# Kernel optimization log

Measured on AMD Instinct MI355X. Metric: run time of the kernel, lower is better.

## Reference

```python
import jax, jax.numpy as jnp
import numpy as np

N = 50000      # nodes
E = 800000     # edges per graph set
D_IN = 128
D_H = 128
NG = 64        # graphs in batch


def gcn(x, W, b, src, dst, w):
    # PyG GCNConv: add self loops (weight 1), symmetric normalization, then
    # out[i] = sum_{(j->i)} norm_ji * (x @ W)[j] + b
    h = x @ W                                   # [N, Dh]
    loop = jnp.arange(N)
    s = jnp.concatenate([src, loop])
    d = jnp.concatenate([dst, loop])
    ww = jnp.concatenate([w, jnp.ones((N,), w.dtype)])
    deg = jax.ops.segment_sum(ww, d, num_segments=N)
    dis = jnp.where(deg > 0, jax.lax.rsqrt(deg), 0.0)
    norm = dis[s] * ww * dis[d]                 # [E+N]
    out = jax.ops.segment_sum(h[s] * norm[:, None], d, num_segments=N)
    return out + b


def setup_inputs() -> dict:
    key = jax.random.key(0)
    ks = jax.random.split(key, 16)
    inp = {
        "edge_index1": jax.random.randint(ks[0], (2, E), 0, N),
        "edge_weight1": jax.random.uniform(ks[1], (E,), jnp.float32),
        "edge_index2": jax.random.randint(ks[2], (2, E), 0, N),
        "edge_weight2": jax.random.uniform(ks[3], (E,), jnp.float32),
        "fm0": jax.random.normal(ks[4], (N, D_IN), jnp.float32),
        "fm1": jax.random.normal(ks[5], (N, D_IN), jnp.float32),
        "batch_tensor": jnp.sort(jax.random.randint(ks[6], (N,), 0, NG)),
        # params (torch Linear stored transposed as [in, out])
        "W1": jax.random.normal(ks[7], (D_IN, D_H), jnp.float32) / np.sqrt(D_IN),
        "b1": jnp.zeros((D_H,), jnp.float32),
        "W2": jax.random.normal(ks[8], (D_H, D_H), jnp.float32) / np.sqrt(D_H),
        "b2": jnp.zeros((D_H,), jnp.float32),
        "M1w": jax.random.normal(ks[9], (D_H, D_H), jnp.float32) / np.sqrt(D_H),
        "M1b": jnp.zeros((D_H,), jnp.float32),
        "M2w": jax.random.normal(ks[10], (D_H, D_H // 2), jnp.float32) / np.sqrt(D_H),
        "M2b": jnp.zeros((D_H // 2,), jnp.float32),
        "M3w": jax.random.normal(ks[11], (D_H // 2, D_H // 4), jnp.float32) / np.sqrt(D_H // 2),
        "M3b": jnp.zeros((D_H // 4,), jnp.float32),
        "M4w": jax.random.normal(ks[12], (D_H // 4, 1), jnp.float32) / np.sqrt(D_H // 4),
        "M4b": jnp.zeros((1,), jnp.float32),
    }
    return inp


def reference(edge_index1, edge_weight1, edge_index2, edge_weight2, fm0, fm1,
              batch_tensor, W1, b1, W2, b2, M1w, M1b, M2w, M2b, M3w, M3b, M4w, M4b):
    s1, d1 = edge_index1[0], edge_index1[1]
    s2, d2 = edge_index2[0], edge_index2[1]
    x11 = gcn(fm0, W1, b1, s1, d1, edge_weight1)
    x12 = gcn(fm1, W1, b1, s2, d2, edge_weight2)
    x21 = gcn(x11, W2, b2, s1, d1, edge_weight1)
    x22 = gcn(x12, W2, b2, s2, d2, edge_weight2)
    x = (x12 - x11) * (x22 - x21)               # [N, Dh]
    # global mean pool by graph id
    sums = jax.ops.segment_sum(x, batch_tensor, num_segments=NG)
    cnt = jax.ops.segment_sum(jnp.ones((N,), x.dtype), batch_tensor, num_segments=NG)
    g = sums / jnp.maximum(cnt, 1.0)[:, None]   # [NG, Dh]
    # MLP (dropout = identity at inference; no activations in original)
    h = g @ M1w + M1b
    h = h @ M2w + M2b
    h = h @ M3w + M3b
    return h @ M4w + M4b                        # [NG, 1]
```

## Files before the change

kernel.cpp:

```cpp
#include <hip/hip_runtime.h>
#include <hip/hip_fp16.h>

#define N_NODES 50000
#define N_EDGES 800000
#define NGRAPH 64
#define PCHUNK 16
#define NRANGE 8
#define RSPAN 6250
#define ECHUNK 2048
#define NCHK ((N_EDGES + ECHUNK - 1) / ECHUNK)
#define AGG_NB 782
#define CAP 48

typedef _Float16 half8 __attribute__((ext_vector_type(8)));
typedef float f32x4 __attribute__((ext_vector_type(4)));

#define GSTRH ((size_t)N_NODES * 128)
#define CCH ((size_t)N_NODES * 32)

__device__ __forceinline__ float pk_w(unsigned p) {
  return __half2float(__ushort_as_half((unsigned short)(p >> 16)));
}
__device__ __forceinline__ unsigned pk_src(unsigned p) { return p & 0xFFFFu; }

__global__ __launch_bounds__(256) void curinit_kernel(
    int* __restrict__ cur1, int* __restrict__ cur2) {
  int i = blockIdx.x * 256 + threadIdx.x;
  if (i < N_NODES) {
    cur1[i] = i * CAP;
    cur2[i] = i * CAP;
  }
}

__global__ __launch_bounds__(256) void fill_kernel(
    const int* __restrict__ ei1, const float* __restrict__ w1,
    int* __restrict__ cur1, unsigned* __restrict__ ec1,
    const int* __restrict__ ei2, const float* __restrict__ w2,
    int* __restrict__ cur2, unsigned* __restrict__ ec2) {
  int r = blockIdx.x & 7, chunk = blockIdx.x >> 3;
  unsigned lo = r * RSPAN;
  int base = chunk * ECHUNK + threadIdx.x;
#pragma unroll
  for (int k = 0; k < ECHUNK / 256; ++k) {
    int e = base + k * 256;
    if (e < N_EDGES) {
      unsigned d1 = (unsigned)__builtin_nontemporal_load(&ei1[N_EDGES + e]);
      if (d1 - lo < RSPAN) {
        int s = __builtin_nontemporal_load(&ei1[e]);
        float w = __builtin_nontemporal_load(&w1[e]);
        int slot = atomicAdd(&cur1[d1], 1);
        if (slot < (int)(d1 * CAP + CAP))
          ec1[slot] = (unsigned)s |
                      ((unsigned)__half_as_ushort(__float2half(w)) << 16);
      }
      unsigned d2 = (unsigned)__builtin_nontemporal_load(&ei2[N_EDGES + e]);
      if (d2 - lo < RSPAN) {
        int s = __builtin_nontemporal_load(&ei2[e]);
        float w = __builtin_nontemporal_load(&w2[e]);
        int slot = atomicAdd(&cur2[d2], 1);
        if (slot < (int)(d2 * CAP + CAP))
          ec2[slot] = (unsigned)s |
                      ((unsigned)__half_as_ushort(__float2half(w)) << 16);
      }
    }
  }
}

__global__ __launch_bounds__(256) void degdis_kernel(
    const int* __restrict__ cn1, const unsigned* __restrict__ ec1,
    const int* __restrict__ cn2, const unsigned* __restrict__ ec2,
    float* __restrict__ dis1, float* __restrict__ dis2) {
  int i = blockIdx.x * 256 + threadIdx.x;
  if (i >= 2 * N_NODES) return;
  const int* cn;
  const unsigned* ec;
  float* dis;
  int node;
  if (i < N_NODES) { cn = cn1; ec = ec1; dis = dis1; node = i; }
  else { cn = cn2; ec = ec2; dis = dis2; node = i - N_NODES; }
  int beg = node * CAP;
  int end = min(cn[node], beg + CAP);
  float s = 1.0f;
  for (int e = beg; e < end; ++e) s += pk_w(ec[e]);
  dis[node] = rsqrtf(s);
}

template <bool XF16>
__global__ __launch_bounds__(256) void gemm_mfma_kernel(
    const void* __restrict__ X0v, const void* __restrict__ X1v,
    const float* __restrict__ W,
    const float* __restrict__ dis1, const float* __restrict__ dis2,
    __half* __restrict__ Y) {
  __shared__ half8 wfrag[4][8][64];
  int tid = threadIdx.x;
  for (int ent = tid; ent < 4 * 8 * 64; ent += 256) {
    int lane = ent & 63, nt = (ent >> 6) & 7, kk = ent >> 9;
    int kbase = kk * 32 + (lane >> 4) * 8;
    int n = nt * 16 + (lane & 15);
    half8 hv;
#pragma unroll
    for (int j = 0; j < 8; ++j) hv[j] = (_Float16)W[(kbase + j) * 128 + n];
    wfrag[kk][nt][lane] = hv;
  }
  __syncthreads();
  int wv = tid >> 6, lane = tid & 63;
  int row0 = blockIdx.x * 64 + wv * 16;
  int arow = row0 + (lane & 15);
  int ar = (arow < 2 * N_NODES) ? arow : 0;
  f32x4 acc[8] = {};
#pragma unroll
  for (int kk = 0; kk < 4; ++kk) {
    int sub = lane >> 4;
    half8 af;
    if constexpr (XF16) {
      int gg = ar >= N_NODES;
      int nd = ar - gg * N_NODES;
      const __half* xs = (const __half*)X0v + (size_t)gg * GSTRH +
                         (size_t)kk * CCH + (size_t)nd * 32 + sub * 8;
      af = *(const half8*)xs;
    } else {
      int kb = kk * 32 + sub * 8;
      const float* xs = (ar < N_NODES)
                            ? ((const float*)X0v + (size_t)ar * 128)
                            : ((const float*)X1v + (size_t)(ar - N_NODES) * 128);
      float4 xa = *(const float4*)(xs + kb);
      float4 xb = *(const float4*)(xs + kb + 4);
      af[0] = (_Float16)xa.x; af[1] = (_Float16)xa.y;
      af[2] = (_Float16)xa.z; af[3] = (_Float16)xa.w;
      af[4] = (_Float16)xb.x; af[5] = (_Float16)xb.y;
      af[6] = (_Float16)xb.z; af[7] = (_Float16)xb.w;
    }
#pragma unroll
    for (int nt = 0; nt < 8; ++nt)
      acc[nt] = __builtin_amdgcn_mfma_f32_16x16x32_f16(af, wfrag[kk][nt][lane],
                                                       acc[nt], 0, 0, 0);
  }
#pragma unroll
  for (int rg = 0; rg < 4; ++rg) {
    int r = row0 + ((lane >> 4) * 4) + rg;
    if (r < 2 * N_NODES) {
      int gg = r >= N_NODES;
      int nd = r - gg * N_NODES;
      float d = gg ? dis2[nd] : dis1[nd];
#pragma unroll
      for (int nt = 0; nt < 8; ++nt)
        Y[(size_t)gg * GSTRH + (size_t)(nt >> 1) * CCH + (size_t)nd * 32 +
          (nt & 1) * 16 + (lane & 15)] = __float2half(d * acc[nt][rg]);
    }
  }
}

__global__ __launch_bounds__(256) void aggregate_kernel(
    const int* __restrict__ cn1, const unsigned* __restrict__ ec1,
    const float* __restrict__ dis1,
    const int* __restrict__ cn2, const unsigned* __restrict__ ec2,
    const float* __restrict__ dis2,
    const __half* __restrict__ H, const float* __restrict__ bias,
    __half* __restrict__ out) {
  int tid = threadIdx.x;
  int combo = blockIdx.x & 7;
  int nb = blockIdx.x >> 3;
  int g = combo >> 2;
  int c = combo & 3;
  int l = tid & 63, w = tid >> 6;
  int node = nb * 64 + w * 16 + (l >> 2);
  int flane = l & 3;
  if (node >= N_NODES) return;
  const int* cn = g ? cn2 : cn1;
  const unsigned* ec = g ? ec2 : ec1;
  const float* dis = g ? dis2 : dis1;
  const float4* T4 = (const float4*)(H + (size_t)g * GSTRH + (size_t)c * CCH);
  float2 a[4];
  a[0] = a[1] = a[2] = a[3] = make_float2(0.f, 0.f);
  int beg = node * CAP;
  int end = min(cn[node], beg + CAP);
  for (int e = beg; e < end; e += 8) {
#pragma unroll
    for (int k = 0; k < 8; ++k) {
      if (e + k < end) {
        unsigned p = ec[e + k];
        float cw = pk_w(p);
        float4 raw = T4[(size_t)pk_src(p) * 4 + flane];
        const __half2* hp = (const __half2*)&raw;
#pragma unroll
        for (int q = 0; q < 4; ++q) {
          float2 hv = __half22float2(hp[q]);
          a[q].x += cw * hv.x;
          a[q].y += cw * hv.y;
        }
      }
    }
  }
  float d = dis[node];
  float4 sraw = T4[(size_t)node * 4 + flane];
  const __half2* sp = (const __half2*)&sraw;
  __half2 o[4];
#pragma unroll
  for (int q = 0; q < 4; ++q) {
    float2 sv = __half22float2(sp[q]);
    float2 bz = *(const float2*)&bias[c * 32 + flane * 8 + q * 2];
    o[q] = __floats2half2_rn(bz.x + d * (sv.x + a[q].x),
                             bz.y + d * (sv.y + a[q].y));
  }
  float4* O4 = (float4*)(out + (size_t)g * GSTRH + (size_t)c * CCH);
  O4[(size_t)node * 4 + flane] = *(float4*)o;
}

__global__ __launch_bounds__(256) void xdiff_kernel(__half* __restrict__ x1) {
  size_t t = (size_t)blockIdx.x * 256 + threadIdx.x;
  const size_t n4 = GSTRH / 8;
  if (t >= n4) return;
  float4* A = (float4*)x1;
  float4 va = A[t];
  float4 vb = A[n4 + t];
  const __half2* pa = (const __half2*)&va;
  const __half2* pb = (const __half2*)&vb;
  __half2 o[4];
#pragma unroll
  for (int q = 0; q < 4; ++q) {
    float2 fa = __half22float2(pa[q]);
    float2 fb = __half22float2(pb[q]);
    o[q] = __floats2half2_rn(fb.x - fa.x, fb.y - fa.y);
  }
  A[t] = *(float4*)o;
}

__global__ __launch_bounds__(256) void pool_diff_kernel(
    const __half* __restrict__ xd,
    const __half* __restrict__ x2,
    const int* __restrict__ batch, float* __restrict__ poolpart) {
  int g = blockIdx.x / PCHUNK, pc = blockIdx.x % PCHUNK;
  int tid = threadIdx.x;
  int lane = tid & 63, grp = lane >> 4, fl = lane & 15;
  int slot = ((tid >> 6) << 2) + grp;
  int cf = fl >> 2, sub = fl & 3;
  int lo, hi;
  { int a = 0, b = N_NODES; while (a < b) { int m = (a + b) >> 1; if (batch[m] < g) a = m + 1; else b = m; } lo = a; }
  { int a = lo, b = N_NODES; while (a < b) { int m = (a + b) >> 1; if (batch[m] < g + 1) a = m + 1; else b = m; } hi = a; }
  int cnt = hi - lo;
  int s = lo + (int)(((long long)cnt * pc) / PCHUNK);
  int e = lo + (int)(((long long)cnt * (pc + 1)) / PCHUNK);
  const float4* D = (const float4*)xd;
  const float4* P = (const float4*)x2;
  size_t db = (size_t)cf * (N_NODES * 4);
  size_t p2b = (size_t)N_NODES * 16 + db;
  float acc[8];
#pragma unroll
  for (int q = 0; q < 8; ++q) acc[q] = 0.f;
  for (int i = s + slot; i < e; i += 16) {
    float4 draw = D[db + (size_t)i * 4 + sub];
    float4 p1raw = P[db + (size_t)i * 4 + sub];
    float4 p2raw = P[p2b + (size_t)i * 4 + sub];
    const __half2* dp = (const __half2*)&draw;
    const __half2* p1p = (const __half2*)&p1raw;
    const __half2* p2p = (const __half2*)&p2raw;
#pragma unroll
    for (int q = 0; q < 4; ++q) {
      float2 dv = __half22float2(dp[q]);
      float2 v1 = __half22float2(p1p[q]);
      float2 v2 = __half22float2(p2p[q]);
      acc[2 * q] += dv.x * (v2.x - v1.x);
      acc[2 * q + 1] += dv.y * (v2.y - v1.y);
    }
  }
  __shared__ float part[16][128];
#pragma unroll
  for (int q = 0; q < 8; ++q) part[slot][cf * 32 + sub * 8 + q] = acc[q];
  __syncthreads();
  if (tid < 128) {
    float s0 = 0.f;
#pragma unroll
    for (int k = 0; k < 16; ++k) s0 += part[k][tid];
    poolpart[(size_t)blockIdx.x * 128 + tid] = s0;
  }
}

__global__ __launch_bounds__(128) void mlp_kernel(
    const float* __restrict__ poolpart, const int* __restrict__ batch,
    const float* __restrict__ M1w, const float* __restrict__ M1b,
    const float* __restrict__ M2w, const float* __restrict__ M2b,
    const float* __restrict__ M3w, const float* __restrict__ M3b,
    const float* __restrict__ M4w, const float* __restrict__ M4b,
    float* __restrict__ out) {
  __shared__ float gv[128], t1[128], t2[64], t3[32];
  const int g = blockIdx.x, j = threadIdx.x;
  int lo, hi;
  { int a = 0, b = N_NODES; while (a < b) { int m = (a + b) >> 1; if (batch[m] < g) a = m + 1; else b = m; } lo = a; }
  { int a = lo, b = N_NODES; while (a < b) { int m = (a + b) >> 1; if (batch[m] < g + 1) a = m + 1; else b = m; } hi = a; }
  float cnt = (float)(hi - lo);
  if (cnt < 1.f) cnt = 1.f;
  float ps = 0.f;
#pragma unroll
  for (int c = 0; c < PCHUNK; ++c)
    ps += poolpart[(size_t)(g * PCHUNK + c) * 128 + j];
  gv[j] = ps / cnt;
  __syncthreads();
  float a = M1b[j];
  for (int k = 0; k < 128; ++k) a += gv[k] * M1w[k * 128 + j];
  t1[j] = a;
  __syncthreads();
  if (j < 64) {
    float b = M2b[j];
    for (int k = 0; k < 128; ++k) b += t1[k] * M2w[k * 64 + j];
    t2[j] = b;
  }
  __syncthreads();
  if (j < 32) {
    float c = M3b[j];
    for (int k = 0; k < 64; ++k) c += t2[k] * M3w[k * 32 + j];
    t3[j] = c;
  }
  __syncthreads();
  if (j == 0) {
    float o = M4b[0];
    for (int k = 0; k < 32; ++k) o += t3[k] * M4w[k];
    out[g] = o;
  }
}

extern "C" void kernel_launch(void* const* d_in, const int* in_sizes, int n_in,
                              void* d_out, int out_size, void* d_ws, size_t ws_size,
                              hipStream_t stream) {
  const int* ei1 = (const int*)d_in[0];
  const float* w1 = (const float*)d_in[1];
  const int* ei2 = (const int*)d_in[2];
  const float* w2 = (const float*)d_in[3];
  const float* fm0 = (const float*)d_in[4];
  const float* fm1 = (const float*)d_in[5];
  const int* batch = (const int*)d_in[6];
  const float* W1 = (const float*)d_in[7];
  const float* b1 = (const float*)d_in[8];
  const float* W2 = (const float*)d_in[9];
  const float* b2 = (const float*)d_in[10];
  const float* M1w = (const float*)d_in[11];
  const float* M1b = (const float*)d_in[12];
  const float* M2w = (const float*)d_in[13];
  const float* M2b = (const float*)d_in[14];
  const float* M3w = (const float*)d_in[15];
  const float* M3b = (const float*)d_in[16];
  const float* M4w = (const float*)d_in[17];
  const float* M4b = (const float*)d_in[18];

  size_t off = 0;
  auto alloc = [&](size_t n) { size_t r = off; off += (n + 15) & ~(size_t)15; return r; };
  size_t o_pool = alloc((size_t)NGRAPH * PCHUNK * 128);
  size_t o_dis1 = alloc(N_NODES);
  size_t o_dis2 = alloc(N_NODES);
  size_t o_cur1 = alloc(N_NODES);
  size_t o_cur2 = alloc(N_NODES);
  size_t o_ec1 = alloc((size_t)N_NODES * CAP);
  size_t o_ec2 = alloc((size_t)N_NODES * CAP);
  size_t o_h = alloc((size_t)N_NODES * 128);
  size_t o_x1 = alloc((size_t)N_NODES * 128);
  size_t o_x2ext = alloc((size_t)N_NODES * 64);
  (void)o_x2ext;
  if (ws_size < off * sizeof(float)) return;

  float* fbase = (float*)d_ws;
  int* ibase = (int*)d_ws;
  float* poolpart = fbase + o_pool;
  float* dis1 = fbase + o_dis1;
  float* dis2 = fbase + o_dis2;
  int* cur1 = ibase + o_cur1;
  int* cur2 = ibase + o_cur2;
  unsigned* ec1 = (unsigned*)(fbase + o_ec1);
  unsigned* ec2 = (unsigned*)(fbase + o_ec2);
  __half* h = (__half*)(fbase + o_h);
  __half* x1h = (__half*)(fbase + o_x1);
  __half* x2h = x1h + GSTRH;

  curinit_kernel<<<(N_NODES + 255) / 256, 256, 0, stream>>>(cur1, cur2);
  fill_kernel<<<NRANGE * NCHK, 256, 0, stream>>>(
      ei1, w1, cur1, ec1, ei2, w2, cur2, ec2);
  degdis_kernel<<<(2 * N_NODES + 255) / 256, 256, 0, stream>>>(
      cur1, ec1, cur2, ec2, dis1, dis2);
  gemm_mfma_kernel<false><<<(2 * N_NODES + 63) / 64, 256, 0, stream>>>(
      fm0, fm1, W1, dis1, dis2, h);
  aggregate_kernel<<<8 * AGG_NB, 256, 0, stream>>>(
      cur1, ec1, dis1, cur2, ec2, dis2, h, b1, x1h);
  gemm_mfma_kernel<true><<<(2 * N_NODES + 63) / 64, 256, 0, stream>>>(
      x1h, nullptr, W2, dis1, dis2, h);
  xdiff_kernel<<<(int)(GSTRH / 8 + 255) / 256, 256, 0, stream>>>(x1h);
  aggregate_kernel<<<8 * AGG_NB, 256, 0, stream>>>(
      cur1, ec1, dis1, cur2, ec2, dis2, h, b2, x2h);
  pool_diff_kernel<<<NGRAPH * PCHUNK, 256, 0, stream>>>(
      x1h, x2h, batch, poolpart);
  mlp_kernel<<<NGRAPH, 128, 0, stream>>>(
      poolpart, batch, M1w, M1b, M2w, M2b, M3w, M3b, M4w, M4b, (float*)d_out);
}
```

Measured before the change: 353.9 us.

## Switch feature buffers from 32-column chunked layout to row-major and regroup aggregation

Replaces the chunked feature layout, where each 32-column slab is stored separately, with plain row-major 128-wide half rows across the GEMM, aggregate and pool kernels. Aggregation now assigns 16 lanes per node so each gathered neighbour row is one contiguous 256-byte read instead of four 64-byte reads in separate blocks. Blocks are interleaved so graph 1 and graph 2 nodes are processed concurrently. Per-edge index loads are now shared across all 128 features rather than repeated per column chunk, at the cost of less cache locality per chunk.

```diff
diff --git a/kernel.cpp b/kernel.cpp
--- a/kernel.cpp
+++ b/kernel.cpp
@@ -9,19 +9,40 @@
 #define RSPAN 6250
 #define ECHUNK 2048
 #define NCHK ((N_EDGES + ECHUNK - 1) / ECHUNK)
-#define AGG_NB 782
+#define AGG_GRID 6256
 #define CAP 48
 
 typedef _Float16 half8 __attribute__((ext_vector_type(8)));
 typedef float f32x4 __attribute__((ext_vector_type(4)));
 
 #define GSTRH ((size_t)N_NODES * 128)
-#define CCH ((size_t)N_NODES * 32)
 
 __device__ __forceinline__ float pk_w(unsigned p) {
   return __half2float(__ushort_as_half((unsigned short)(p >> 16)));
 }
 __device__ __forceinline__ unsigned pk_src(unsigned p) { return p & 0xFFFFu; }
+
+__device__ __forceinline__ void edge_gather_g16(
+    const unsigned* __restrict__ ec, int beg, int end,
+    const float4* __restrict__ Hb4, int fl, float2 a[4]) {
+  for (int e = beg; e < end; e += 8) {
+#pragma unroll
+    for (int k = 0; k < 8; ++k) {
+      if (e + k < end) {
+        unsigned p = ec[e + k];
+        float c = pk_w(p);
+        float4 raw = Hb4[(size_t)pk_src(p) * 16 + fl];
+        const __half2* hp = (const __half2*)&raw;
+#pragma unroll
+        for (int q = 0; q < 4; ++q) {
+          float2 hv = __half22float2(hp[q]);
+          a[q].x += c * hv.x;
+          a[q].y += c * hv.y;
+        }
+      }
+    }
+  }
+}
 
 __global__ __launch_bounds__(256) void curinit_kernel(
     int* __restrict__ cur1, int* __restrict__ cur2) {
@@ -110,16 +131,14 @@
   f32x4 acc[8] = {};
 #pragma unroll
   for (int kk = 0; kk < 4; ++kk) {
-    int sub = lane >> 4;
+    int kb = kk * 32 + (lane >> 4) * 8;
     half8 af;
     if constexpr (XF16) {
-      int gg = ar >= N_NODES;
-      int nd = ar - gg * N_NODES;
-      const __half* xs = (const __half*)X0v + (size_t)gg * GSTRH +
-                         (size_t)kk * CCH + (size_t)nd * 32 + sub * 8;
-      af = *(const half8*)xs;
+      const __half* xs = (ar < N_NODES)
+                             ? ((const __half*)X0v + (size_t)ar * 128)
+                             : ((const __half*)X1v + (size_t)(ar - N_NODES) * 128);
+      af = *(const half8*)(xs + kb);
     } else {
-      int kb = kk * 32 + sub * 8;
       const float* xs = (ar < N_NODES)
                             ? ((const float*)X0v + (size_t)ar * 128)
                             : ((const float*)X1v + (size_t)(ar - N_NODES) * 128);
@@ -139,13 +158,10 @@
   for (int rg = 0; rg < 4; ++rg) {
     int r = row0 + ((lane >> 4) * 4) + rg;
     if (r < 2 * N_NODES) {
-      int gg = r >= N_NODES;
-      int nd = r - gg * N_NODES;
-      float d = gg ? dis2[nd] : dis1[nd];
+      float d = (r < N_NODES) ? dis1[r] : dis2[r - N_NODES];
 #pragma unroll
       for (int nt = 0; nt < 8; ++nt)
-        Y[(size_t)gg * GSTRH + (size_t)(nt >> 1) * CCH + (size_t)nd * 32 +
-          (nt & 1) * 16 + (lane & 15)] = __float2half(d * acc[nt][rg]);
+        Y[(size_t)r * 128 + nt * 16 + (lane & 15)] = __float2half(d * acc[nt][rg]);
     }
   }
 }
@@ -158,52 +174,41 @@
     const __half* __restrict__ H, const float* __restrict__ bias,
     __half* __restrict__ out) {
   int tid = threadIdx.x;
-  int combo = blockIdx.x & 7;
-  int nb = blockIdx.x >> 3;
-  int g = combo >> 2;
-  int c = combo & 3;
-  int l = tid & 63, w = tid >> 6;
-  int node = nb * 64 + w * 16 + (l >> 2);
-  int flane = l & 3;
-  if (node >= N_NODES) return;
-  const int* cn = g ? cn2 : cn1;
-  const unsigned* ec = g ? ec2 : ec1;
-  const float* dis = g ? dis2 : dis1;
-  const float4* T4 = (const float4*)(H + (size_t)g * GSTRH + (size_t)c * CCH);
+  int lane = tid & 63, grp = lane >> 4, fl = lane & 15;
+  int bid = blockIdx.x;
+  int r = bid & 7, c = bid >> 3;
+  int wb = (r < 4) ? (c * 4 + r) : (AGG_GRID / 2 + c * 4 + (r - 4));
+  int idx = wb * 16 + ((tid >> 6) << 2) + grp;
+  if (idx >= 2 * N_NODES) return;
+  const int* cn;
+  const unsigned* ec;
+  const float* dis;
+  const float4* Hb4;
+  int node;
+  if (idx < N_NODES) {
+    cn = cn1; ec = ec1; dis = dis1; node = idx;
+    Hb4 = (const float4*)H;
+  } else {
+    cn = cn2; ec = ec2; dis = dis2; node = idx - N_NODES;
+    Hb4 = (const float4*)(H + GSTRH);
+  }
   float2 a[4];
   a[0] = a[1] = a[2] = a[3] = make_float2(0.f, 0.f);
   int beg = node * CAP;
   int end = min(cn[node], beg + CAP);
-  for (int e = beg; e < end; e += 8) {
-#pragma unroll
-    for (int k = 0; k < 8; ++k) {
-      if (e + k < end) {
-        unsigned p = ec[e + k];
-        float cw = pk_w(p);
-        float4 raw = T4[(size_t)pk_src(p) * 4 + flane];
-        const __half2* hp = (const __half2*)&raw;
-#pragma unroll
-        for (int q = 0; q < 4; ++q) {
-          float2 hv = __half22float2(hp[q]);
-          a[q].x += cw * hv.x;
-          a[q].y += cw * hv.y;
-        }
-      }
-    }
-  }
+  edge_gather_g16(ec, beg, end, Hb4, fl, a);
   float d = dis[node];
-  float4 sraw = T4[(size_t)node * 4 + flane];
+  float4 sraw = Hb4[(size_t)node * 16 + fl];
   const __half2* sp = (const __half2*)&sraw;
   __half2 o[4];
 #pragma unroll
   for (int q = 0; q < 4; ++q) {
     float2 sv = __half22float2(sp[q]);
-    float2 bz = *(const float2*)&bias[c * 32 + flane * 8 + q * 2];
+    float2 bz = *(const float2*)&bias[fl * 8 + q * 2];
     o[q] = __floats2half2_rn(bz.x + d * (sv.x + a[q].x),
                              bz.y + d * (sv.y + a[q].y));
   }
-  float4* O4 = (float4*)(out + (size_t)g * GSTRH + (size_t)c * CCH);
-  O4[(size_t)node * 4 + flane] = *(float4*)o;
+  *(float4*)&out[(size_t)idx * 128 + fl * 8] = *(float4*)o;
 }
 
 __global__ __launch_bounds__(256) void xdiff_kernel(__half* __restrict__ x1) {
@@ -233,7 +238,6 @@
   int tid = threadIdx.x;
   int lane = tid & 63, grp = lane >> 4, fl = lane & 15;
   int slot = ((tid >> 6) << 2) + grp;
-  int cf = fl >> 2, sub = fl & 3;
   int lo, hi;
   { int a = 0, b = N_NODES; while (a < b) { int m = (a + b) >> 1; if (batch[m] < g) a = m + 1; else b = m; } lo = a; }
   { int a = lo, b = N_NODES; while (a < b) { int m = (a + b) >> 1; if (batch[m] < g + 1) a = m + 1; else b = m; } hi = a; }
@@ -242,15 +246,14 @@
   int e = lo + (int)(((long long)cnt * (pc + 1)) / PCHUNK);
   const float4* D = (const float4*)xd;
   const float4* P = (const float4*)x2;
-  size_t db = (size_t)cf * (N_NODES * 4);
-  size_t p2b = (size_t)N_NODES * 16 + db;
+  const size_t offB = (size_t)N_NODES * 16;
   float acc[8];
 #pragma unroll
   for (int q = 0; q < 8; ++q) acc[q] = 0.f;
   for (int i = s + slot; i < e; i += 16) {
-    float4 draw = D[db + (size_t)i * 4 + sub];
-    float4 p1raw = P[db + (size_t)i * 4 + sub];
-    float4 p2raw = P[p2b + (size_t)i * 4 + sub];
+    float4 draw = D[(size_t)i * 16 + fl];
+    float4 p1raw = P[(size_t)i * 16 + fl];
+    float4 p2raw = P[offB + (size_t)i * 16 + fl];
     const __half2* dp = (const __half2*)&draw;
     const __half2* p1p = (const __half2*)&p1raw;
     const __half2* p2p = (const __half2*)&p2raw;
@@ -265,7 +268,7 @@
   }
   __shared__ float part[16][128];
 #pragma unroll
-  for (int q = 0; q < 8; ++q) part[slot][cf * 32 + sub * 8 + q] = acc[q];
+  for (int q = 0; q < 8; ++q) part[slot][fl * 8 + q] = acc[q];
   __syncthreads();
   if (tid < 128) {
     float s0 = 0.f;
@@ -376,12 +379,12 @@
       cur1, ec1, cur2, ec2, dis1, dis2);
   gemm_mfma_kernel<false><<<(2 * N_NODES + 63) / 64, 256, 0, stream>>>(
       fm0, fm1, W1, dis1, dis2, h);
-  aggregate_kernel<<<8 * AGG_NB, 256, 0, stream>>>(
+  aggregate_kernel<<<AGG_GRID, 256, 0, stream>>>(
       cur1, ec1, dis1, cur2, ec2, dis2, h, b1, x1h);
   gemm_mfma_kernel<true><<<(2 * N_NODES + 63) / 64, 256, 0, stream>>>(
-      x1h, nullptr, W2, dis1, dis2, h);
+      x1h, x1h + GSTRH, W2, dis1, dis2, h);
   xdiff_kernel<<<(int)(GSTRH / 8 + 255) / 256, 256, 0, stream>>>(x1h);
-  aggregate_kernel<<<8 * AGG_NB, 256, 0, stream>>>(
+  aggregate_kernel<<<AGG_GRID, 256, 0, stream>>>(
       cur1, ec1, dis1, cur2, ec2, dis2, h, b2, x2h);
   pool_diff_kernel<<<NGRAPH * PCHUNK, 256, 0, stream>>>(
       x1h, x2h, batch, poolpart);
```

New measurement: 313.9 us, median of 2. 1.13x faster.
